# Kernel optimization log

Hardware: AMD Instinct MI355X
Metric: run time of the kernel (lower is better)

The kernel has to match this reference:

```python
import jax, jax.numpy as jnp
import numpy as np

B_SZ, SEQ = 2, 4096
D_MODEL, D_STATE, D_CONV, HEADDIM = 768, 128, 4, 64
D_INNER = 1536
NHEADS = D_INNER // HEADDIM  # 24
D_XBC = D_INNER + 2 * D_STATE  # 1792
D_PROJ = 2 * D_INNER + 2 * D_STATE + NHEADS  # 3352
CHUNK = 128
EPS = 1e-5


def setup_inputs():
    key = jax.random.key(0)
    ks = jax.random.split(key, 10)
    feature = jax.random.normal(ks[0], (B_SZ, SEQ, D_MODEL), jnp.float32)
    in_proj_w = jax.random.normal(ks[1], (D_PROJ, D_MODEL), jnp.float32) * 0.02
    conv_w = jax.random.normal(ks[2], (D_XBC, D_CONV), jnp.float32) * 0.2
    conv_b = jax.random.normal(ks[3], (D_XBC,), jnp.float32) * 0.02
    dt_bias = jnp.log(jnp.expm1(jax.random.uniform(ks[4], (NHEADS,), jnp.float32, 0.001, 0.1)))
    A_log = jnp.log(jax.random.uniform(ks[5], (NHEADS,), jnp.float32, 1.0, 16.0))
    D = jax.random.normal(ks[6], (NHEADS,), jnp.float32) * 0.1 + 1.0
    norm_w = jnp.ones((D_INNER,), jnp.float32)
    out_proj_w = jax.random.normal(ks[7], (D_MODEL, D_INNER), jnp.float32) * 0.02
    gate1 = jnp.float32(0.6)
    return {"feature": feature, "gate1": gate1, "in_proj_w": in_proj_w, "conv_w": conv_w,
            "conv_b": conv_b, "dt_bias": dt_bias, "A_log": A_log, "D": D,
            "norm_w": norm_w, "out_proj_w": out_proj_w}


def segsum(x):
    # x: (..., T) -> (..., T, T); out[..., i, j] = sum_{k=j+1..i} x[..., k]; -inf above diagonal
    T = x.shape[-1]
    xc = jnp.cumsum(x, axis=-1)
    d = xc[..., :, None] - xc[..., None, :]
    mask = jnp.tril(jnp.ones((T, T), bool))
    return jnp.where(mask, d, -jnp.inf)


def ssd(xd, Adt, B, C):
    # Chunked SSD (Mamba2 selective scan). xd: (b,L,H,P) = x*dt; Adt: (b,L,H); B,C: (b,L,N)
    b, L, H, P = xd.shape
    c, Q = L // CHUNK, CHUNK
    xd = xd.reshape(b, c, Q, H, P)
    Adt = Adt.reshape(b, c, Q, H).transpose(0, 3, 1, 2)          # (b,H,c,Q)
    Bc = B.reshape(b, c, Q, -1)
    Cc = C.reshape(b, c, Q, -1)
    A_cum = jnp.cumsum(Adt, axis=-1)                             # (b,H,c,Q)
    Lmat = jnp.exp(segsum(Adt))                                  # (b,H,c,Q,Q)
    CB = jnp.einsum('bcln,bcsn->bcls', Cc, Bc)                   # (b,c,Q,Q)
    Y_diag = jnp.einsum('bcls,bhcls,bcshp->bclhp', CB, Lmat, xd)
    decay_states = jnp.exp(A_cum[..., -1:] - A_cum)              # (b,H,c,Q)
    states = jnp.einsum('bcln,bhcl,bclhp->bchpn', Bc, decay_states, xd)  # (b,c,H,P,N)
    A_last = A_cum[..., -1]                                      # (b,H,c)
    decay_chunk = jnp.exp(segsum(jnp.pad(A_last, ((0, 0), (0, 0), (1, 0)))))  # (b,H,c+1,c+1)
    states_pad = jnp.concatenate([jnp.zeros_like(states[:, :1]), states], axis=1)
    prev = jnp.einsum('bhzc,bchpn->bzhpn', decay_chunk, states_pad)[:, :-1]   # state at chunk start
    Y_off = jnp.einsum('bcln,bhcl,bchpn->bclhp', Cc, jnp.exp(A_cum), prev)
    return (Y_diag + Y_off).reshape(b, L, H, P)


def reference(feature, gate1, in_proj_w, conv_w, conv_b, dt_bias, A_log, D, norm_w, out_proj_w):
    b, L, _ = feature.shape
    zxbcdt = feature @ in_proj_w.T                               # (b,L,3352)
    z = zxbcdt[..., :D_INNER]
    xBC = zxbcdt[..., D_INNER:D_INNER + D_XBC]
    dt = jax.nn.softplus(zxbcdt[..., -NHEADS:] + dt_bias)       # (b,L,H)
    # causal depthwise conv1d (kernel=4) + SiLU
    xp = jnp.pad(xBC, ((0, 0), (D_CONV - 1, 0), (0, 0)))
    xconv = sum(conv_w[:, k] * xp[:, k:k + L, :] for k in range(D_CONV)) + conv_b
    xBC = jax.nn.silu(xconv)
    x = xBC[..., :D_INNER].reshape(b, L, NHEADS, HEADDIM)
    Bm = xBC[..., D_INNER:D_INNER + D_STATE]
    Cm = xBC[..., D_INNER + D_STATE:]
    A = -jnp.exp(A_log)                                          # (H,)
    y = ssd(x * dt[..., None], dt * A, Bm, Cm) + D[:, None] * x  # skip term D*x
    y = y.reshape(b, L, D_INNER)
    # gated RMSNorm (norm_before_gate=False): gate first, then rmsnorm
    y = y * jax.nn.silu(z)
    y = y * jax.lax.rsqrt(jnp.mean(y * y, axis=-1, keepdims=True) + EPS) * norm_w
    out = y @ out_proj_w.T                                       # out_proj (bias=False)
    return jax.nn.sigmoid(gate1) * out + feature
```

## Files before the change

### kernel.cpp

```cpp
#include <hip/hip_runtime.h>
#include <hip/hip_bf16.h>
#include <math.h>

#define B_SZ 2
#define SEQ 4096
#define DMODEL 768
#define DSTATE 128
#define HEADDIM 64
#define DINNER 1536
#define NHEADS 24
#define DXBC 1792
#define DPROJ 3352
#define NPAD1 3456
#define CHUNK 128
#define NCHUNK 32
#define ROWS (B_SZ*SEQ)
#define LDTC 136
#define LDE 136
#define LDE2 132
#define LDEY 65

typedef float floatx4 __attribute__((ext_vector_type(4)));
typedef __bf16 bf16x8 __attribute__((ext_vector_type(8)));

__device__ __forceinline__ float sigmoidf_(float x){ return 1.f/(1.f+__expf(-x)); }
__device__ __forceinline__ float siluf_(float x){ return x/(1.f+__expf(-x)); }
__device__ __forceinline__ float softplusf_(float x){ return (x>20.f)? x : __logf(1.f+__expf(x)); }
__device__ __forceinline__ __bf16 cvt_bf(float x){ __hip_bfloat16 t = __float2bfloat16(x); return *(__bf16*)&t; }

__device__ __forceinline__ void gload_lds16(const __hip_bfloat16* g, __hip_bfloat16* l){
    __builtin_amdgcn_global_load_lds(
        (const __attribute__((address_space(1))) void*)g,
        (__attribute__((address_space(3))) void*)l, 16, 0, 0);
}

__global__ __launch_bounds__(512)
void gemm1_mfma(const __hip_bfloat16* __restrict__ A,
                const __hip_bfloat16* __restrict__ W,
                __hip_bfloat16* __restrict__ z16, __hip_bfloat16* __restrict__ xbc16,
                float* __restrict__ dtb, const float* __restrict__ dt_bias)
{
    __shared__ __align__(16) char smem[49152];
    __hip_bfloat16* Asm = (__hip_bfloat16*)smem;
    __hip_bfloat16* Wsm = Asm + 256*64;
    const int tid = threadIdx.x;
    const int lane = tid & 63, wave = tid >> 6;
    const int blk = blockIdx.x;
    const int m_tile = ((blk & 7) << 2) | ((blk >> 3) & 3);
    const int bx = blk >> 5;
    const int bm = m_tile*256, bn = bx*128;
    const int wm = (wave & 3)*64, wn = (wave >> 2)*64;
    const int r16 = lane & 15, qbase = lane >> 4, sw = r16 & 7;
    floatx4 acc[4][4] = {};
    for (int k0 = 0; k0 < DMODEL; k0 += 64) {
#pragma unroll
        for (int j = 0; j < 4; ++j) {
            int cc = j*512 + tid;
            int row = cc >> 3, jc = cc & 7;
            int sj = jc ^ (row & 7);
            gload_lds16(A + (size_t)(bm+row)*DMODEL + k0 + sj*8, Asm + cc*8);
        }
#pragma unroll
        for (int j = 0; j < 2; ++j) {
            int cc = j*512 + tid;
            int row = cc >> 3, jc = cc & 7;
            int sj = jc ^ (row & 7);
            gload_lds16(W + (size_t)(bn+row)*DMODEL + k0 + sj*8, Wsm + cc*8);
        }
        __syncthreads();
#pragma unroll
        for (int ks = 0; ks < 2; ++ks) {
            const int kq = ((qbase + ks*4) ^ sw)*8;
            bf16x8 af[4], wf[4];
#pragma unroll
            for (int i = 0; i < 4; ++i) {
                af[i] = *(const bf16x8*)(Asm + (wm + i*16 + r16)*64 + kq);
                wf[i] = *(const bf16x8*)(Wsm + (wn + i*16 + r16)*64 + kq);
            }
#pragma unroll
            for (int mi = 0; mi < 4; ++mi)
#pragma unroll
                for (int ni = 0; ni < 4; ++ni)
                    acc[mi][ni] = __builtin_amdgcn_mfma_f32_16x16x32_bf16(
                        af[mi], wf[ni], acc[mi][ni], 0, 0, 0);
        }
        __syncthreads();
    }
    const int col = lane & 15, rowq = (lane >> 4)*4;
    if (bx == 26) {
        if (wn == 0) {
#pragma unroll
            for (int mi = 0; mi < 4; ++mi)
#pragma unroll
                for (int ni = 0; ni < 2; ++ni) {
                    int h = ni*16 + col;
                    if (h < NHEADS)
#pragma unroll
                        for (int r = 0; r < 4; ++r) {
                            int m = bm + wm + mi*16 + rowq + r;
                            dtb[(size_t)m*NHEADS + h] =
                                softplusf_(acc[mi][ni][r] + dt_bias[h]);
                        }
                }
        }
        return;
    }
    __hip_bfloat16* Tsm = (__hip_bfloat16*)smem;
    __hip_bfloat16* dst; int ldd;
    if (bx < 12) { dst = z16 + bn;            ldd = DINNER; }
    else         { dst = xbc16 + bn - DINNER; ldd = DXBC;  }
    for (int half = 0; half < 2; ++half) {
        if (((wave & 3) >> 1) == half) {
#pragma unroll
            for (int mi = 0; mi < 4; ++mi)
#pragma unroll
                for (int ni = 0; ni < 4; ++ni)
#pragma unroll
                    for (int r = 0; r < 4; ++r)
                        Tsm[(wm - half*128 + mi*16 + rowq + r)*LDE + wn + ni*16 + col] =
                            __float2bfloat16(acc[mi][ni][r]);
        }
        __syncthreads();
#pragma unroll
        for (int it = 0; it < 4; ++it) {
            int e = it*512 + tid;
            int row = e >> 4, c0 = (e & 15)*8;
            bf16x8 v = *(const bf16x8*)(Tsm + row*LDE + c0);
            *(bf16x8*)(dst + (size_t)(bm + half*128 + row)*ldd + c0) = v;
        }
        __syncthreads();
    }
}

__global__ __launch_bounds__(256)
void gemm2_mfma(const __hip_bfloat16* __restrict__ A,
                const __hip_bfloat16* __restrict__ W,
                float* __restrict__ C,
                const float* __restrict__ gate, const float* __restrict__ resid,
                const float* __restrict__ rowsq)
{
    __shared__ __align__(16) char smem[33792];
    __shared__ float scale_lds[128];
    __hip_bfloat16* Asm = (__hip_bfloat16*)smem;
    __hip_bfloat16* Wsm = Asm + 128*64;
    const int tid = threadIdx.x;
    const int lane = tid & 63, wave = tid >> 6;
    const int blk = blockIdx.x;
    const int mblk = blk & 63;
    const int m_tile = ((mblk & 7) << 3) | (mblk >> 3);
    const int bm = m_tile*128, bn = (blk >> 6)*128;
    const int wm = (wave & 1)*64, wn = (wave >> 1)*64;
    const int r16 = lane & 15, qbase = lane >> 4, sw = r16 & 7;
    floatx4 acc[4][4] = {};
    for (int k0 = 0; k0 < DINNER; k0 += 64) {
#pragma unroll
        for (int j = 0; j < 4; ++j) {
            int cc = j*256 + tid;
            int row = cc >> 3, jc = cc & 7;
            int sj = jc ^ (row & 7);
            gload_lds16(A + (size_t)(bm+row)*DINNER + k0 + sj*8, Asm + cc*8);
        }
#pragma unroll
        for (int j = 0; j < 4; ++j) {
            int cc = j*256 + tid;
            int row = cc >> 3, jc = cc & 7;
            int sj = jc ^ (row & 7);
            gload_lds16(W + (size_t)(bn+row)*DINNER + k0 + sj*8, Wsm + cc*8);
        }
        __syncthreads();
#pragma unroll
        for (int ks = 0; ks < 2; ++ks) {
            const int kq = ((qbase + ks*4) ^ sw)*8;
            bf16x8 af[4], wf[4];
#pragma unroll
            for (int i = 0; i < 4; ++i) {
                af[i] = *(const bf16x8*)(Asm + (wm + i*16 + r16)*64 + kq);
                wf[i] = *(const bf16x8*)(Wsm + (wn + i*16 + r16)*64 + kq);
            }
#pragma unroll
            for (int mi = 0; mi < 4; ++mi)
#pragma unroll
                for (int ni = 0; ni < 4; ++ni)
                    acc[mi][ni] = __builtin_amdgcn_mfma_f32_16x16x32_bf16(
                        af[mi], wf[ni], acc[mi][ni], 0, 0, 0);
        }
        __syncthreads();
    }
    if (tid < 128)
        scale_lds[tid] = rsqrtf(rowsq[bm + tid] * (1.f/DINNER) + 1e-5f);
    float gs = sigmoidf_(gate[0]);
    __syncthreads();
    const int col = lane & 15, rowq = (lane >> 4)*4;
    float* Tsm = (float*)smem;
    for (int half = 0; half < 2; ++half) {
        if ((wave & 1) == half) {
#pragma unroll
            for (int mi = 0; mi < 4; ++mi)
#pragma unroll
                for (int ni = 0; ni < 4; ++ni)
#pragma unroll
                    for (int r = 0; r < 4; ++r)
                        Tsm[(mi*16 + rowq + r)*LDE2 + wn + ni*16 + col] = acc[mi][ni][r];
        }
        __syncthreads();
#pragma unroll
        for (int it = 0; it < 8; ++it) {
            int e = it*256 + tid;
            int row = e >> 5, c0 = (e & 31)*4;
            float4 v = *(const float4*)(Tsm + row*LDE2 + c0);
            float sc = gs * scale_lds[half*64 + row];
            size_t off = (size_t)(bm + half*64 + row)*DMODEL + bn + c0;
            float4 rv = *(const float4*)(resid + off);
            v.x = sc*v.x + rv.x; v.y = sc*v.y + rv.y;
            v.z = sc*v.z + rv.z; v.w = sc*v.w + rv.w;
            *(float4*)(C + off) = v;
        }
        __syncthreads();
    }
}

#define NC1 (ROWS*DMODEL)
#define NC2 (NPAD1*DMODEL)
#define NC3 (DMODEL*DINNER)
#define NV1 (NC1/8)
#define NV2 (NC2/8)
#define NV3 (NC3/8)
#define NVR (ROWS/8)
__global__ __launch_bounds__(256)
void cast_all(const float* __restrict__ feature, const float* __restrict__ in_w,
              const float* __restrict__ out_w, const float* __restrict__ nw,
              __hip_bfloat16* __restrict__ fbf, __hip_bfloat16* __restrict__ wbf,
              __hip_bfloat16* __restrict__ owbf, float* __restrict__ rowsq)
{
    int v = blockIdx.x*256 + threadIdx.x;
    if (v < NV1) {
        int i = v*8;
        float4 a = *(const float4*)(feature + i);
        float4 b = *(const float4*)(feature + i + 4);
        bf16x8 o;
        o[0]=cvt_bf(a.x); o[1]=cvt_bf(a.y); o[2]=cvt_bf(a.z); o[3]=cvt_bf(a.w);
        o[4]=cvt_bf(b.x); o[5]=cvt_bf(b.y); o[6]=cvt_bf(b.z); o[7]=cvt_bf(b.w);
        *(bf16x8*)(fbf + i) = o;
    } else if (v < NV1 + NV2) {
        int j = (v - NV1)*8;
        int n = j / DMODEL, k = j - n*DMODEL;
        bf16x8 o;
        if (n < DPROJ) {
            const float* s = in_w + (size_t)n*DMODEL + k;
            float4 a = *(const float4*)(s);
            float4 b = *(const float4*)(s + 4);
            o[0]=cvt_bf(a.x); o[1]=cvt_bf(a.y); o[2]=cvt_bf(a.z); o[3]=cvt_bf(a.w);
            o[4]=cvt_bf(b.x); o[5]=cvt_bf(b.y); o[6]=cvt_bf(b.z); o[7]=cvt_bf(b.w);
        } else {
#pragma unroll
            for (int q = 0; q < 8; ++q) o[q] = (__bf16)0.f;
        }
        *(bf16x8*)(wbf + j) = o;
    } else if (v < NV1 + NV2 + NV3) {
        int j = (v - NV1 - NV2)*8;
        int k = j % DINNER;
        float4 a  = *(const float4*)(out_w + j);
        float4 b  = *(const float4*)(out_w + j + 4);
        float4 na = *(const float4*)(nw + k);
        float4 nb = *(const float4*)(nw + k + 4);
        bf16x8 o;
        o[0]=cvt_bf(a.x*na.x); o[1]=cvt_bf(a.y*na.y); o[2]=cvt_bf(a.z*na.z); o[3]=cvt_bf(a.w*na.w);
        o[4]=cvt_bf(b.x*nb.x); o[5]=cvt_bf(b.y*nb.y); o[6]=cvt_bf(b.z*nb.z); o[7]=cvt_bf(b.w*nb.w);
        *(bf16x8*)(owbf + j) = o;
    } else if (v < NV1 + NV2 + NV3 + NVR) {
        int j = (v - NV1 - NV2 - NV3)*8;
        float4 z = {0.f, 0.f, 0.f, 0.f};
        *(float4*)(rowsq + j) = z;
        *(float4*)(rowsq + j + 4) = z;
    }
}

__global__ __launch_bounds__(512)
void conv_scan_k(const __hip_bfloat16* __restrict__ xbc16, const float* __restrict__ cw,
                 const float* __restrict__ cbias,
                 __hip_bfloat16* __restrict__ x_t,
                 __hip_bfloat16* __restrict__ B_n, __hip_bfloat16* __restrict__ B_t,
                 __hip_bfloat16* __restrict__ C_n,
                 const float* __restrict__ dtb, const float* __restrict__ A_log,
                 float* __restrict__ acum)
{
    int xb = blockIdx.x;
    int tid = threadIdx.x;
    if (xb >= 14) {
        __shared__ float wtot;
        int h = xb - 14, c = blockIdx.y, b = blockIdx.z;
        int lane = tid & 63;
        float s = 0.f;
        if (tid < 128) {
            float Aa = -__expf(A_log[h]);
            s = dtb[((size_t)b*SEQ + c*CHUNK + tid)*NHEADS + h] * Aa;
#pragma unroll
            for (int off = 1; off < 64; off <<= 1) {
                float t = __shfl_up(s, off);
                if (lane >= off) s += t;
            }
            if (tid == 63) wtot = s;
        }
        __syncthreads();
        if (tid >= 64 && tid < 128) s += wtot;
        if (tid < 128)
            acum[((b*NHEADS+h)*NCHUNK + c)*CHUNK + tid] = s;
        return;
    }
    __shared__ __align__(16) __hip_bfloat16 in[131*LDTC];
    int ct = xb, lt = blockIdx.y, b = blockIdx.z;
    int base = lt*128;
    for (int it = 0; it < 2096; it += 512) {
        int e = it + tid; if (e >= 2096) break;
        int row = e >> 4, c0 = (e & 15)*8;
        int l = base - 3 + row;
        bf16x8 v;
        if (l < 0) { for (int j = 0; j < 8; ++j) v[j] = (__bf16)0.f; }
        else v = *(const bf16x8*)(xbc16 + ((size_t)b*SEQ + l)*DXBC + ct*128 + c0);
        *(bf16x8*)(in + row*LDTC + c0) = v;
    }
    __syncthreads();
    int ch = tid & 127, lh = tid >> 7, l0 = lh*32;
    int g = ct*128 + ch;
    float w0 = cw[g*4+0], w1 = cw[g*4+1], w2 = cw[g*4+2], w3 = cw[g*4+3];
    float bias = cbias[g];
    float a0 = __bfloat162float(in[(l0+0)*LDTC + ch]);
    float a1 = __bfloat162float(in[(l0+1)*LDTC + ch]);
    float a2 = __bfloat162float(in[(l0+2)*LDTC + ch]);
    size_t trow = 0;
    if (ct < 12)      trow = ((size_t)b*NHEADS + (g>>6))*HEADDIM + (g & 63);
    else if (ct == 12) trow = (size_t)b*DSTATE + ch;
    bf16x8 obuf;
#pragma unroll
    for (int li = 0; li < 32; ++li) {
        float a3 = __bfloat162float(in[(l0+li+3)*LDTC + ch]);
        float o = siluf_(bias + w0*a0 + w1*a1 + w2*a2 + w3*a3);
        a0 = a1; a1 = a2; a2 = a3;
        __hip_bfloat16 ob = __float2bfloat16(o);
        size_t rr = (size_t)b*SEQ + base + l0 + li;
        if (ct == 12)      B_n[rr*DSTATE + ch] = ob;
        else if (ct == 13) C_n[rr*DSTATE + ch] = ob;
        obuf[li & 7] = *(const __bf16*)&ob;
        if ((li & 7) == 7 && ct <= 12) {
            __hip_bfloat16* dst = (ct < 12) ? x_t : B_t;
            *(bf16x8*)(dst + trow*SEQ + base + l0 + (li - 7)) = obuf;
        }
    }
}

__global__ __launch_bounds__(256)
void cbst_k(const __hip_bfloat16* __restrict__ B_n, const __hip_bfloat16* __restrict__ C_n,
            __hip_bfloat16* __restrict__ CB16,
            const __hip_bfloat16* __restrict__ x_t, const __hip_bfloat16* __restrict__ B_t,
            const float* __restrict__ dtb, const float* __restrict__ acum,
            __hip_bfloat16* __restrict__ states)
{
    int bid = blockIdx.x;
    int tid = threadIdx.x, lane = tid & 63, wave = tid >> 6;
    if (bid < 64) {
        int c = bid & 31, b = bid >> 5;
        size_t base = (size_t)b*SEQ + c*CHUNK;
        int r16 = lane & 15, kq = (lane>>4)*8;
        floatx4 acc[2][8] = {};
#pragma unroll
        for (int ks = 0; ks < 4; ++ks) {
            int k0 = ks*32 + kq;
            bf16x8 af[2], bfv[8];
#pragma unroll
            for (int mt = 0; mt < 2; ++mt)
                af[mt] = *(const bf16x8*)(C_n + (base + (wave*2+mt)*16 + r16)*DSTATE + k0);
#pragma unroll
            for (int st = 0; st < 8; ++st)
                bfv[st] = *(const bf16x8*)(B_n + (base + st*16 + r16)*DSTATE + k0);
#pragma unroll
            for (int mt = 0; mt < 2; ++mt)
#pragma unroll
                for (int st = 0; st < 8; ++st)
                    if (st <= wave*2+mt)
                        acc[mt][st] = __builtin_amdgcn_mfma_f32_16x16x32_bf16(
                            af[mt], bfv[st], acc[mt][st], 0,0,0);
        }
        size_t cbb = (size_t)(b*NCHUNK+c)*CHUNK*CHUNK;
        int scol = lane & 15, rowq = (lane>>4)*4;
#pragma unroll
        for (int mt = 0; mt < 2; ++mt)
#pragma unroll
            for (int st = 0; st < 8; ++st)
                if (st <= wave*2+mt)
#pragma unroll
                    for (int r = 0; r < 4; ++r)
                        CB16[cbb + (size_t)((wave*2+mt)*16 + rowq + r)*CHUNK + st*16 + scol] =
                            __float2bfloat16(acc[mt][st][r]);
        return;
    }
    __shared__ float f[128];
    int t = bid - 64;
    int c = t & 31;
    int h = (t>>5) % NHEADS;
    int b = t/(32*NHEADS);
    int arow = ((b*NHEADS+h)*NCHUNK + c)*CHUNK;
    size_t rbase = (size_t)b*SEQ + c*CHUNK;
    if (tid < 128) {
        float alast = acum[arow + 127];
        f[tid] = dtb[(rbase + tid)*NHEADS + h] * __expf(alast - acum[arow + tid]);
    }
    __syncthreads();
    int r16 = lane & 15, kq = (lane>>4)*8;
    size_t xtb = ((size_t)b*NHEADS + h)*HEADDIM;
    int cl = c*CHUNK;
    floatx4 acc[8] = {};
#pragma unroll
    for (int ks = 0; ks < 4; ++ks) {
        int k0 = ks*32 + kq;
        bf16x8 xa = *(const bf16x8*)(x_t + (xtb + wave*16 + r16)*SEQ + cl + k0);
        bf16x8 af;
#pragma unroll
        for (int j = 0; j < 8; ++j)
            af[j] = (__bf16)((float)xa[j] * f[k0 + j]);
        bf16x8 bfv[8];
#pragma unroll
        for (int nt = 0; nt < 8; ++nt)
            bfv[nt] = *(const bf16x8*)(B_t + ((size_t)b*DSTATE + nt*16 + r16)*SEQ + cl + k0);
#pragma unroll
        for (int nt = 0; nt < 8; ++nt)
            acc[nt] = __builtin_amdgcn_mfma_f32_16x16x32_bf16(af, bfv[nt], acc[nt], 0,0,0);
    }
    size_t sb = ((size_t)(b*NCHUNK+c)*NHEADS + h)*(HEADDIM*DSTATE);
    int ncol = lane & 15, rowq = (lane>>4)*4;
#pragma unroll
    for (int nt = 0; nt < 8; ++nt)
#pragma unroll
        for (int r = 0; r < 4; ++r)
            states[sb + (size_t)(wave*16 + rowq + r)*DSTATE + nt*16 + ncol] =
                __float2bfloat16(acc[nt][r]);
}

__global__ __launch_bounds__(64)
void recur_k(__hip_bfloat16* __restrict__ states, const float* __restrict__ acum)
{
    int pb = blockIdx.x & 15;
    int bh = blockIdx.x >> 4;
    int h = bh % NHEADS, b = bh / NHEADS;
    int voff = (pb*64 + threadIdx.x)*8;
    const size_t cstride = (size_t)NHEADS*HEADDIM*DSTATE;
    size_t base0 = ((size_t)(b*NCHUNK)*NHEADS + h)*(HEADDIM*DSTATE) + voff;
    bf16x8 st[NCHUNK];
    float ev[NCHUNK];
#pragma unroll
    for (int c = 0; c < NCHUNK; ++c)
        st[c] = *(const bf16x8*)(states + base0 + (size_t)c*cstride);
#pragma unroll
    for (int c = 0; c < NCHUNK; ++c)
        ev[c] = __expf(acum[((b*NHEADS+h)*NCHUNK + c)*CHUNK + 127]);
    float S[8] = {};
#pragma unroll
    for (int c = 0; c < NCHUNK; ++c) {
        bf16x8 pv;
#pragma unroll
        for (int j = 0; j < 8; ++j) {
            pv[j] = (__bf16)S[j];
            S[j] = S[j]*ev[c] + (float)st[c][j];
        }
        *(bf16x8*)(states + base0 + (size_t)c*cstride) = pv;
    }
}

__global__ __launch_bounds__(512, 4)
void y_mfma(const __hip_bfloat16* __restrict__ x_t, const __hip_bfloat16* __restrict__ z16,
            const __hip_bfloat16* __restrict__ C_n, const __hip_bfloat16* __restrict__ CB16,
            const __hip_bfloat16* __restrict__ states, const float* __restrict__ dtb,
            const float* __restrict__ acum, const float* __restrict__ Dp,
            __hip_bfloat16* __restrict__ y16, float* __restrict__ rowsq)
{
    __shared__ __align__(16) char smem[32768];
    __hip_bfloat16* XT = (__hip_bfloat16*)smem;
    __hip_bfloat16* ST = XT + 64*128;
    __shared__ __align__(16) float Tsm[128*LDEY];
    __shared__ float ac[128], dts[128], gk[128];
    const int tid = threadIdx.x, lane = tid & 63, wave = tid >> 6;
    const int r16 = lane & 15, kq = (lane>>4)*8;
    const int l = wave*16 + r16;
    const int pcol = lane & 15, rowq = (lane>>4)*4;
    const int erow = tid >> 2, ec0 = (tid & 3)*16;
    const int NU = B_SZ*NHEADS*NCHUNK;
    {
        int u = blockIdx.x;
        int c = u & 31, h = (u>>5) % NHEADS, b = u/(32*NHEADS);
        size_t xtb = ((size_t)b*NHEADS + h)*HEADDIM;
        size_t sb  = ((size_t)(b*NCHUNK+c)*NHEADS + h)*(HEADDIM*DSTATE);
        int cl = c*CHUNK;
#pragma unroll
        for (int j = 0; j < 2; ++j) {
            int cc = j*512 + tid;
            int p = cc >> 4, ch = cc & 15;
            int sj = ch ^ (p & 7);
            gload_lds16(x_t + (xtb + p)*SEQ + cl + sj*8, XT + cc*8);
            gload_lds16(states + sb + (size_t)p*DSTATE + sj*8, ST + cc*8);
        }
    }
#pragma unroll 1
    for (int u = blockIdx.x; u < NU; u += 512) {
        int c = u & 31;
        int h = (u>>5) % NHEADS;
        int b = u/(32*NHEADS);
        int arow = ((b*NHEADS+h)*NCHUNK + c)*CHUNK;
        size_t rbase = (size_t)b*SEQ + c*CHUNK;
        size_t cbb = (size_t)(b*NCHUNK+c)*CHUNK*CHUNK;
        if (tid < 128) {
            ac[tid]  = acum[arow + tid];
            dts[tid] = dtb[(rbase + tid)*NHEADS + h];
        }
        __syncthreads();
        if (tid < 128)
            gk[tid] = __expf(ac[tid & 96] - ac[tid]) * dts[tid];
        bf16x8 cb[4], cv[4];
#pragma unroll
        for (int ks = 0; ks < 4; ++ks) {
            cb[ks] = *(const bf16x8*)(CB16 + cbb + (size_t)l*CHUNK + ks*32 + kq);
            cv[ks] = *(const bf16x8*)(C_n + (rbase + l)*DSTATE + ks*32 + kq);
        }
        bf16x8 zA = *(const bf16x8*)(z16 + (rbase + erow)*DINNER + h*HEADDIM + ec0);
        bf16x8 zB = *(const bf16x8*)(z16 + (rbase + erow)*DINNER + h*HEADDIM + ec0 + 8);
        __syncthreads();
        float acl = ac[l];
        float Dh = Dp[h];
        floatx4 acc[4] = {};
        int nks = (wave >> 1) + 1;
#pragma unroll
        for (int ks = 0; ks < 4; ++ks) {
            if (ks < nks) {
                int k0 = ks*32 + kq;
                float fl = __expf(acl - ac[ks*32]);
                bf16x8 af;
#pragma unroll
                for (int j = 0; j < 8; ++j) {
                    int s = k0 + j;
                    float w = (s <= l) ? (float)cb[ks][j] * (fl * gk[s]) : 0.f;
                    if (s == l) w += Dh;
                    af[j] = (__bf16)w;
                }
                int chL = k0 >> 3;
                bf16x8 bfv[4];
#pragma unroll
                for (int pt = 0; pt < 4; ++pt) {
                    int row = pt*16 + r16;
                    bfv[pt] = *(const bf16x8*)(XT + (row*16 + (chL ^ (row & 7)))*8);
                }
#pragma unroll
                for (int pt = 0; pt < 4; ++pt)
                    acc[pt] = __builtin_amdgcn_mfma_f32_16x16x32_bf16(af, bfv[pt], acc[pt], 0,0,0);
            }
        }
        float eal = __expf(acl);
#pragma unroll
        for (int ks = 0; ks < 4; ++ks) {
            int k0 = ks*32 + kq;
            bf16x8 af;
#pragma unroll
            for (int j = 0; j < 8; ++j)
                af[j] = (__bf16)((float)cv[ks][j] * eal);
            int chL = k0 >> 3;
            bf16x8 bfv[4];
#pragma unroll
            for (int pt = 0; pt < 4; ++pt) {
                int row = pt*16 + r16;
                bfv[pt] = *(const bf16x8*)(ST + (row*16 + (chL ^ (row & 7)))*8);
            }
#pragma unroll
            for (int pt = 0; pt < 4; ++pt)
                acc[pt] = __builtin_amdgcn_mfma_f32_16x16x32_bf16(af, bfv[pt], acc[pt], 0,0,0);
        }
        __syncthreads();
        int un = u + 512;
        if (un < NU) {
            int c2 = un & 31, h2 = (un>>5) % NHEADS, b2 = un/(32*NHEADS);
            size_t xtb2 = ((size_t)b2*NHEADS + h2)*HEADDIM;
            size_t sb2  = ((size_t)(b2*NCHUNK+c2)*NHEADS + h2)*(HEADDIM*DSTATE);
            int cl2 = c2*CHUNK;
#pragma unroll
            for (int j = 0; j < 2; ++j) {
                int cc = j*512 + tid;
                int p = cc >> 4, ch = cc & 15;
                int sj = ch ^ (p & 7);
                gload_lds16(x_t + (xtb2 + p)*SEQ + cl2 + sj*8, XT + cc*8);
                gload_lds16(states + sb2 + (size_t)p*DSTATE + sj*8, ST + cc*8);
            }
        }
#pragma unroll
        for (int pt = 0; pt < 4; ++pt)
#pragma unroll
            for (int r = 0; r < 4; ++r)
                Tsm[(wave*16 + rowq + r)*LDEY + pt*16 + pcol] = acc[pt][r];
        __syncthreads();
        {
            float s = 0.f; bf16x8 o1, o2;
#pragma unroll
            for (int j2 = 0; j2 < 8; ++j2) {
                float g = Tsm[erow*LDEY + ec0 + j2] * siluf_(__bfloat162float(zA[j2]));
                o1[j2] = cvt_bf(g); s += g*g;
            }
#pragma unroll
            for (int j2 = 0; j2 < 8; ++j2) {
                float g = Tsm[erow*LDEY + ec0 + 8 + j2] * siluf_(__bfloat162float(zB[j2]));
                o2[j2] = cvt_bf(g); s += g*g;
            }
            size_t grow = rbase + erow;
            *(bf16x8*)(y16 + grow*DINNER + h*HEADDIM + ec0)     = o1;
            *(bf16x8*)(y16 + grow*DINNER + h*HEADDIM + ec0 + 8) = o2;
            s += __shfl_xor(s, 1); s += __shfl_xor(s, 2);
            if ((tid & 3) == 0)
                atomicAdd(rowsq + grow, s);
        }
    }
}

extern "C" void kernel_launch(void* const* d_in, const int* in_sizes, int n_in,
                              void* d_out, int out_size, void* d_ws, size_t ws_size,
                              hipStream_t stream)
{
    const float* feature = (const float*)d_in[0];
    const float* gate1   = (const float*)d_in[1];
    const float* in_w    = (const float*)d_in[2];
    const float* conv_w  = (const float*)d_in[3];
    const float* conv_b  = (const float*)d_in[4];
    const float* dt_bias = (const float*)d_in[5];
    const float* A_log   = (const float*)d_in[6];
    const float* Dp      = (const float*)d_in[7];
    const float* norm_w  = (const float*)d_in[8];
    const float* out_w   = (const float*)d_in[9];
    float* out = (float*)d_out;

    char* p = (char*)d_ws;
    __hip_bfloat16* z16   = (__hip_bfloat16*)p; p += (size_t)ROWS*DINNER*2;
    __hip_bfloat16* xbc16 = (__hip_bfloat16*)p; p += (size_t)ROWS*DXBC*2;
    __hip_bfloat16* x_t   = (__hip_bfloat16*)p; p += (size_t)ROWS*DINNER*2;
    __hip_bfloat16* B_n   = (__hip_bfloat16*)p; p += (size_t)ROWS*DSTATE*2;
    __hip_bfloat16* B_t   = (__hip_bfloat16*)p; p += (size_t)ROWS*DSTATE*2;
    __hip_bfloat16* C_n   = (__hip_bfloat16*)p; p += (size_t)ROWS*DSTATE*2;
    float* dtb    = (float*)p;            p += (size_t)ROWS*NHEADS*4;
    float* acum   = (float*)p;            p += (size_t)B_SZ*NHEADS*NCHUNK*CHUNK*4;
    float* rowsq  = (float*)p;            p += (size_t)ROWS*4;
    __hip_bfloat16* CB16 = (__hip_bfloat16*)p; p += (size_t)B_SZ*NCHUNK*CHUNK*CHUNK*2;
    __hip_bfloat16* states = (__hip_bfloat16*)p; p += (size_t)B_SZ*NCHUNK*NHEADS*HEADDIM*DSTATE*2;
    __hip_bfloat16* y16  = (__hip_bfloat16*)p; p += (size_t)ROWS*DINNER*2;
    __hip_bfloat16* fbf  = (__hip_bfloat16*)p; p += (size_t)ROWS*DMODEL*2;
    __hip_bfloat16* wbf  = (__hip_bfloat16*)p; p += (size_t)NPAD1*DMODEL*2;
    __hip_bfloat16* owbf = (__hip_bfloat16*)p; p += (size_t)DMODEL*DINNER*2;

    cast_all<<<(NV1+NV2+NV3+NVR+255)/256, 256, 0, stream>>>(feature, in_w, out_w, norm_w,
                                                            fbf, wbf, owbf, rowsq);

    gemm1_mfma<<<27*32, 512, 0, stream>>>(fbf, wbf, z16, xbc16, dtb, dt_bias);
    conv_scan_k<<<dim3(14 + NHEADS, 32, B_SZ), 512, 0, stream>>>(
        xbc16, conv_w, conv_b, x_t, B_n, B_t, C_n, dtb, A_log, acum);
    cbst_k<<<64 + B_SZ*NHEADS*NCHUNK, 256, 0, stream>>>(
        B_n, C_n, CB16, x_t, B_t, dtb, acum, states);
    recur_k<<<B_SZ*NHEADS*16, 64, 0, stream>>>(states, acum);
    y_mfma<<<512, 512, 0, stream>>>(x_t, z16, C_n, CB16, states,
                                    dtb, acum, Dp, y16, rowsq);
    gemm2_mfma<<<6*64, 256, 0, stream>>>(y16, owbf, out, gate1, feature, rowsq);
}
```

Before: 277.4 us.

## Stage transposed conv outputs and B tile through LDS for coalesced access

After: 264.1 us. 1.05x faster.

```diff
diff --git a/kernel.cpp b/kernel.cpp
--- a/kernel.cpp
+++ b/kernel.cpp
@@ -16,6 +16,7 @@
 #define NCHUNK 32
 #define ROWS (B_SZ*SEQ)
 #define LDTC 136
+#define LDTT 132
 #define LDE 136
 #define LDE2 132
 #define LDEY 65
@@ -308,6 +309,7 @@
         return;
     }
     __shared__ __align__(16) __hip_bfloat16 in[131*LDTC];
+    __shared__ __align__(16) __hip_bfloat16 T[128*LDTT];
     int ct = xb, lt = blockIdx.y, b = blockIdx.z;
     int base = lt*128;
     for (int it = 0; it < 2096; it += 512) {
@@ -327,10 +329,6 @@
     float a0 = __bfloat162float(in[(l0+0)*LDTC + ch]);
     float a1 = __bfloat162float(in[(l0+1)*LDTC + ch]);
     float a2 = __bfloat162float(in[(l0+2)*LDTC + ch]);
-    size_t trow = 0;
-    if (ct < 12)      trow = ((size_t)b*NHEADS + (g>>6))*HEADDIM + (g & 63);
-    else if (ct == 12) trow = (size_t)b*DSTATE + ch;
-    bf16x8 obuf;
 #pragma unroll
     for (int li = 0; li < 32; ++li) {
         float a3 = __bfloat162float(in[(l0+li+3)*LDTC + ch]);
@@ -340,10 +338,22 @@
         size_t rr = (size_t)b*SEQ + base + l0 + li;
         if (ct == 12)      B_n[rr*DSTATE + ch] = ob;
         else if (ct == 13) C_n[rr*DSTATE + ch] = ob;
-        obuf[li & 7] = *(const __bf16*)&ob;
-        if ((li & 7) == 7 && ct <= 12) {
-            __hip_bfloat16* dst = (ct < 12) ? x_t : B_t;
-            *(bf16x8*)(dst + trow*SEQ + base + l0 + (li - 7)) = obuf;
+        if (ct <= 12)
+            T[ch*LDTT + l0 + li] = ob;
+    }
+    if (ct <= 12) {
+        __syncthreads();
+        __hip_bfloat16* dst = (ct < 12) ? x_t : B_t;
+#pragma unroll
+        for (int it = 0; it < 4; ++it) {
+            int e = it*512 + tid;
+            int chn = e >> 4, c0 = (e & 15)*8;
+            int g2 = ct*128 + chn;
+            size_t trow = (ct < 12)
+                ? ((size_t)b*NHEADS + (g2>>6))*HEADDIM + (g2 & 63)
+                : (size_t)b*DSTATE + chn;
+            bf16x8 v = *(const bf16x8*)(T + chn*LDTT + c0);
+            *(bf16x8*)(dst + trow*SEQ + base + c0) = v;
         }
     }
 }
@@ -355,6 +365,8 @@
             const float* __restrict__ dtb, const float* __restrict__ acum,
             __hip_bfloat16* __restrict__ states)
 {
+    __shared__ __align__(16) __hip_bfloat16 BT[128*128];
+    __shared__ float f[128];
     int bid = blockIdx.x;
     int tid = threadIdx.x, lane = tid & 63, wave = tid >> 6;
     if (bid < 64) {
@@ -393,13 +405,20 @@
                             __float2bfloat16(acc[mt][st][r]);
         return;
     }
-    __shared__ float f[128];
     int t = bid - 64;
     int c = t & 31;
     int h = (t>>5) % NHEADS;
     int b = t/(32*NHEADS);
     int arow = ((b*NHEADS+h)*NCHUNK + c)*CHUNK;
     size_t rbase = (size_t)b*SEQ + c*CHUNK;
+    int cl = c*CHUNK;
+#pragma unroll
+    for (int j = 0; j < 8; ++j) {
+        int cc = j*256 + tid;
+        int n = cc >> 4, chk = cc & 15;
+        int sj = chk ^ (n & 7);
+        gload_lds16(B_t + ((size_t)b*DSTATE + n)*SEQ + cl + sj*8, BT + cc*8);
+    }
     if (tid < 128) {
         float alast = acum[arow + 127];
         f[tid] = dtb[(rbase + tid)*NHEADS + h] * __expf(alast - acum[arow + tid]);
@@ -407,7 +426,6 @@
     __syncthreads();
     int r16 = lane & 15, kq = (lane>>4)*8;
     size_t xtb = ((size_t)b*NHEADS + h)*HEADDIM;
-    int cl = c*CHUNK;
     floatx4 acc[8] = {};
 #pragma unroll
     for (int ks = 0; ks < 4; ++ks) {
@@ -417,10 +435,13 @@
 #pragma unroll
         for (int j = 0; j < 8; ++j)
             af[j] = (__bf16)((float)xa[j] * f[k0 + j]);
+        int chL = k0 >> 3;
         bf16x8 bfv[8];
 #pragma unroll
-        for (int nt = 0; nt < 8; ++nt)
-            bfv[nt] = *(const bf16x8*)(B_t + ((size_t)b*DSTATE + nt*16 + r16)*SEQ + cl + k0);
+        for (int nt = 0; nt < 8; ++nt) {
+            int row = nt*16 + r16;
+            bfv[nt] = *(const bf16x8*)(BT + (row*16 + (chL ^ (row & 7)))*8);
+        }
 #pragma unroll
         for (int nt = 0; nt < 8; ++nt)
             acc[nt] = __builtin_amdgcn_mfma_f32_16x16x32_bf16(af, bfv[nt], acc[nt], 0,0,0);
```
